# Performance work log

Hardware: AMD Instinct MI355X
Metric: run time of the kernel (lower is better)

Reference implementation:

```python
import jax, jax.numpy as jnp
import numpy as np

BETA = 0.25
B, N, D = 8, 4096, 256
NUM_CODES = 4096


def setup_inputs() -> dict:
    key = jax.random.key(0)
    kx, kc = jax.random.split(key)
    x = jax.random.normal(kx, (B, N, D), dtype=jnp.float32)
    # matches nn.init.uniform_(weight, -1/dim, 1/dim)
    codebook = jax.random.uniform(kc, (NUM_CODES, D), dtype=jnp.float32,
                                  minval=-1.0 / D, maxval=1.0 / D)
    return {"x": x, "codebook": codebook}


def reference(x, codebook):
    b, n, d = x.shape
    flat = x.reshape(b * n, d)                                   # [BN, D]
    # squared euclidean distances: ||z||^2 - 2 z.e^T + ||e||^2   # [BN, K]
    distances = (jnp.sum(flat * flat, axis=1, keepdims=True)
                 - 2.0 * jnp.einsum('md,kd->mk', flat, codebook)
                 + jnp.sum(codebook * codebook, axis=1)[None, :])
    indices = jnp.argmin(distances, axis=1)                      # [BN]
    z_q = codebook[indices].reshape(b, n, d)                     # [B, N, D]
    # commitment + codebook losses (detach == stop_gradient)
    sg = jax.lax.stop_gradient
    loss = jnp.mean((sg(z_q) - x) ** 2) + BETA * jnp.mean((z_q - sg(x)) ** 2)
    # straight-through estimator
    z_q_st = x + sg(z_q - x)
    return z_q_st, loss, indices.reshape(b, n)
```

## Files before the change

kernel.cpp:

```cpp
#include <hip/hip_runtime.h>

#define MTOT 32768
#define KC   4096
#define DDIM 256
#define BM   64
#define ZELEMS (MTOT * DDIM)
#define THRESH 2.0e-4f
#define WLCAP 8192
#define RGRID 2048

typedef _Float16 half8 __attribute__((ext_vector_type(8)));
typedef float f32x4 __attribute__((ext_vector_type(4)));

__device__ __forceinline__ void gload_lds16(const void* g, void* l) {
  __builtin_amdgcn_global_load_lds(
      (const __attribute__((address_space(1))) void*)g,
      (__attribute__((address_space(3))) void*)l, 16, 0, 0);
}

__device__ __forceinline__ float sqr_rn(float v) { return __fmul_rn(v, v); }

__global__ __launch_bounds__(256) void vq_prep2(const float* __restrict__ x,
                                                const float* __restrict__ cb,
                                                float* __restrict__ S,
                                                float* __restrict__ cnorm,
                                                _Float16* __restrict__ cbsw,
                                                int* __restrict__ wl_count,
                                                double* __restrict__ accum) {
  const int t = threadIdx.x;
  if (blockIdx.x == 0 && t == 0) { *accum = 0.0; *wl_count = 0; }
  const int sub = t >> 4, lane16 = t & 15;
  const int h = lane16 >> 3, j = lane16 & 7;
  const bool isrow = blockIdx.x < 2048;
  const int idx = (isrow ? blockIdx.x : blockIdx.x - 2048) * 16 + sub;
  const float* p = (isrow ? x + (size_t)idx * DDIM : cb + (size_t)idx * DDIM);

  float r = 0.f;
  const float* q = p + h * 128 + j;
#pragma unroll
  for (int i = 0; i < 16; ++i) r = __fadd_rn(r, sqr_rn(q[i * 8]));
  r = __fadd_rn(r, __shfl_xor(r, 1, 64));
  r = __fadd_rn(r, __shfl_xor(r, 2, 64));
  r = __fadd_rn(r, __shfl_xor(r, 4, 64));
  float sv = __fadd_rn(r, __shfl_xor(r, 8, 64));
  if (lane16 == 0) {
    if (isrow) S[idx] = sv; else cnorm[idx] = sv;
  }

  if (!isrow) {
    const int sw = idx & 7;
    _Float16* dst = cbsw + (size_t)idx * DDIM;
#pragma unroll
    for (int c = 0; c < 2; ++c) {
      int jj = lane16 + c * 16;
      float4 a4 = *reinterpret_cast<const float4*>(p + jj * 8);
      float4 b4 = *reinterpret_cast<const float4*>(p + jj * 8 + 4);
      union { half8 v; _Float16 hh[8]; } u;
      u.hh[0] = (_Float16)(a4.x * 256.0f); u.hh[1] = (_Float16)(a4.y * 256.0f);
      u.hh[2] = (_Float16)(a4.z * 256.0f); u.hh[3] = (_Float16)(a4.w * 256.0f);
      u.hh[4] = (_Float16)(b4.x * 256.0f); u.hh[5] = (_Float16)(b4.y * 256.0f);
      u.hh[6] = (_Float16)(b4.z * 256.0f); u.hh[7] = (_Float16)(b4.w * 256.0f);
      *reinterpret_cast<half8*>(dst + ((jj ^ sw) * 8)) = u.v;
    }
  }
}

__global__ __launch_bounds__(256, 2) void vq_score(const float* __restrict__ x,
                                                   const _Float16* __restrict__ cbsw,
                                                   const float* __restrict__ Sarr,
                                                   const float* __restrict__ cnorm,
                                                   int* __restrict__ bestidx,
                                                   int* __restrict__ wl,
                                                   int* __restrict__ wl_count,
                                                   double* __restrict__ accum) {
  __shared__ _Float16 cbt[4][2][4096];
  __shared__ float scrV1[4][BM];
  __shared__ float scrV2[4][BM];
  __shared__ int   scrI1[4][BM];

  const int t = threadIdx.x;
  const int m0 = blockIdx.x * BM;
  const int lane = t & 63, w = t >> 6;
  const int lo = lane & 15, hi = lane >> 4;

#pragma unroll
  for (int j = 0; j < 8; ++j)
    gload_lds16(cbsw + w * 4096 + j * 512 + lane * 8, &cbt[w][0][j * 512]);

  half8 a[4][8];
#pragma unroll
  for (int s2 = 0; s2 < 4; ++s2) {
    const float* xr = x + (size_t)(m0 + s2 * 16 + lo) * DDIM + hi * 8;
#pragma unroll
    for (int s = 0; s < 8; ++s) {
      float4 u0 = *reinterpret_cast<const float4*>(xr + s * 32);
      float4 u1 = *reinterpret_cast<const float4*>(xr + s * 32 + 4);
      union { half8 v; _Float16 h[8]; } uu;
      uu.h[0] = (_Float16)u0.x; uu.h[1] = (_Float16)u0.y;
      uu.h[2] = (_Float16)u0.z; uu.h[3] = (_Float16)u0.w;
      uu.h[4] = (_Float16)u1.x; uu.h[5] = (_Float16)u1.y;
      uu.h[6] = (_Float16)u1.z; uu.h[7] = (_Float16)u1.w;
      a[s2][s] = uu.v;
    }
  }

  const int code_l = w * 16 + lo;
  const int bswz = (lo & 7) << 3;

  float v1[4][4], v2[4][4]; int i1[4][4];
#pragma unroll
  for (int s2 = 0; s2 < 4; ++s2)
#pragma unroll
    for (int r = 0; r < 4; ++r) { v1[s2][r] = 3.4e38f; v2[s2][r] = 3.4e38f; i1[s2][r] = 0; }

  float Ccur = cnorm[code_l];

  for (int kt = 0; kt < KC / 64; ++kt) {
#pragma unroll
    for (int s2 = 0; s2 < 4; ++s2)
#pragma unroll
      for (int s = 0; s < 8; ++s)
        asm volatile("" : "+v"(a[s2][s]));

    const int cur = kt & 1;
    asm volatile("s_waitcnt vmcnt(0) lgkmcnt(0)" ::: "memory");
    if (kt < KC / 64 - 1) {
      const _Float16* src = cbsw + (size_t)(kt + 1) * 16384 + w * 4096 + lane * 8;
#pragma unroll
      for (int j = 0; j < 8; ++j)
        gload_lds16(src + j * 512, &cbt[w][cur ^ 1][j * 512]);
    }
    float Cnext = (kt < KC / 64 - 1) ? cnorm[(kt + 1) * 64 + code_l] : 0.f;

    f32x4 acc[4];
#pragma unroll
    for (int s2 = 0; s2 < 4; ++s2) acc[s2] = (f32x4){0.f, 0.f, 0.f, 0.f};
#pragma unroll
    for (int s = 0; s < 8; ++s) {
      half8 b = *reinterpret_cast<half8*>(
          &cbt[w][cur][(lo * 256 + s * 32 + hi * 8) ^ bswz]);
      acc[0] = __builtin_amdgcn_mfma_f32_16x16x32_f16(a[0][s], b, acc[0], 0, 0, 0);
      acc[1] = __builtin_amdgcn_mfma_f32_16x16x32_f16(a[1][s], b, acc[1], 0, 0, 0);
      acc[2] = __builtin_amdgcn_mfma_f32_16x16x32_f16(a[2][s], b, acc[2], 0, 0, 0);
      acc[3] = __builtin_amdgcn_mfma_f32_16x16x32_f16(a[3][s], b, acc[3], 0, 0, 0);
    }
    const int code = kt * 64 + code_l;
#pragma unroll
    for (int s2 = 0; s2 < 4; ++s2) {
#pragma unroll
      for (int r = 0; r < 4; ++r) {
        float sv = fmaf(acc[s2][r], -0.0078125f, Ccur);
        bool lt = sv < v1[s2][r];
        v2[s2][r] = fminf(v2[s2][r], lt ? v1[s2][r] : sv);
        if (lt) { v1[s2][r] = sv; i1[s2][r] = code; }
      }
    }
    Ccur = Cnext;
  }

#pragma unroll
  for (int s2 = 0; s2 < 4; ++s2) {
#pragma unroll
    for (int r = 0; r < 4; ++r) {
      float v = v1[s2][r], u = v2[s2][r]; int ii = i1[s2][r];
#pragma unroll
      for (int m = 1; m <= 8; m <<= 1) {
        float ov = __shfl_xor(v, m, 64);
        int   oi = __shfl_xor(ii, m, 64);
        float ou = __shfl_xor(u, m, 64);
        float mx = fmaxf(v, ov);
        u = fminf(fminf(u, ou), mx);
        bool take = (ov < v) || (ov == v && oi < ii);
        if (take) { v = ov; ii = oi; }
      }
      if (lo == 0) {
        int rowl = s2 * 16 + hi * 4 + r;
        scrV1[w][rowl] = v;
        scrV2[w][rowl] = u;
        scrI1[w][rowl] = ii;
      }
    }
  }
  __syncthreads();

  float part = 0.f;
  if (t < BM) {
    float bv1 = 3.4e38f, bv2 = 3.4e38f; int bi1 = 0x7fffffff;
#pragma unroll
    for (int c = 0; c < 4; ++c) {
      float v = scrV1[c][t];
      float u = scrV2[c][t];
      int  ii = scrI1[c][t];
      float mx = fmaxf(bv1, v);
      bv2 = fminf(fminf(bv2, u), mx);
      if (v < bv1 || (v == bv1 && ii < bi1)) { bv1 = v; bi1 = ii; }
    }
    int row = m0 + t;
    bestidx[row] = bi1;
    float gap = bv2 - bv1;
    if (gap <= THRESH) {
      int pos = atomicAdd(wl_count, 1);
      if (pos >= WLCAP) part = __fadd_rn(Sarr[row], bv1);
      else wl[pos] = row;
    } else {
      part = __fadd_rn(Sarr[row], bv1);
    }
  }
#pragma unroll
  for (int off = 32; off >= 1; off >>= 1) part += __shfl_down(part, off, 64);
  if (t == 0) atomicAdd(accum, (double)part);
}

__global__ __launch_bounds__(256) void vq_rescore(const float* __restrict__ x,
                                                  const float* __restrict__ cb,
                                                  const float* __restrict__ Sarr,
                                                  const float* __restrict__ cnorm,
                                                  const int* __restrict__ wl,
                                                  const int* __restrict__ wl_count,
                                                  float* __restrict__ pD,
                                                  int* __restrict__ pI) {
  const int cnt = min(*wl_count, WLCAP);
  if (cnt == 0) return;
  const int ngroups = (cnt + 3) >> 2;
  const int nitems = ngroups * 16;

  __shared__ float xs[4][260];
  __shared__ int rsh[4];
  __shared__ float scrv[4][4];
  __shared__ int   scri[4][4];

  const int t = threadIdx.x;
  const int lane = t & 63, w = t >> 6;

  for (int item = blockIdx.x; item < nitems; item += RGRID) {
    const int g = item >> 4, chunk = item & 15;
    __syncthreads();
    if (t < 4) { int e = g * 4 + t; rsh[t] = wl[(e < cnt) ? e : g * 4]; }
    __syncthreads();
    { int i = t >> 6, dq = t & 63;
      *reinterpret_cast<float4*>(&xs[i][dq * 4]) =
          *reinterpret_cast<const float4*>(x + (size_t)rsh[i] * DDIM + dq * 4); }
    __syncthreads();

    const int code = chunk * 256 + t;
    const float* cp = cb + (size_t)code * DDIM;
    const float C = cnorm[code];

    float acc[4][4];
#pragma unroll
    for (int i = 0; i < 4; ++i)
#pragma unroll
      for (int l = 0; l < 4; ++l) acc[i][l] = 0.f;

#pragma unroll 8
    for (int dq = 0; dq < 64; ++dq) {
      float4 cv = *reinterpret_cast<const float4*>(cp + dq * 4);
#pragma unroll
      for (int i = 0; i < 4; ++i) {
        float4 xv = *reinterpret_cast<float4*>(&xs[i][dq * 4]);
        acc[i][0] = __fadd_rn(acc[i][0], __fmul_rn(xv.x, cv.x));
        acc[i][1] = __fadd_rn(acc[i][1], __fmul_rn(xv.y, cv.y));
        acc[i][2] = __fadd_rn(acc[i][2], __fmul_rn(xv.z, cv.z));
        acc[i][3] = __fadd_rn(acc[i][3], __fmul_rn(xv.w, cv.w));
      }
    }

#pragma unroll
    for (int i = 0; i < 4; ++i) {
      float e = __fadd_rn(__fadd_rn(acc[i][0], acc[i][1]),
                          __fadd_rn(acc[i][2], acc[i][3]));
      float Sv = Sarr[rsh[i]];
      float D = __fadd_rn(__fsub_rn(Sv, __fmul_rn(2.0f, e)), C);
      float v = D; int ii = code;
#pragma unroll
      for (int m = 1; m <= 32; m <<= 1) {
        float ov = __shfl_xor(v, m, 64);
        int   oi = __shfl_xor(ii, m, 64);
        if (ov < v || (ov == v && oi < ii)) { v = ov; ii = oi; }
      }
      if (lane == 0) { scrv[i][w] = v; scri[i][w] = ii; }
    }
    __syncthreads();
    if (t < 4) {
      float bv = 3.4e38f; int bi = 0x7fffffff;
#pragma unroll
      for (int c = 0; c < 4; ++c) {
        float v = scrv[t][c]; int ii = scri[t][c];
        if (v < bv || (v == bv && ii < bi)) { bv = v; bi = ii; }
      }
      int rpos = g * 4 + t;
      if (rpos < cnt) { pD[rpos * 16 + chunk] = bv; pI[rpos * 16 + chunk] = bi; }
    }
  }
}

__global__ __launch_bounds__(256) void vq_combine(const int* __restrict__ wl,
                                                  const int* __restrict__ wl_count,
                                                  const float* __restrict__ pD,
                                                  const int* __restrict__ pI,
                                                  int* __restrict__ bestidx,
                                                  double* __restrict__ accum) {
  const int cnt = min(*wl_count, WLCAP);
  for (int r = blockIdx.x * 256 + threadIdx.x; r < cnt; r += gridDim.x * 256) {
    float bv = 3.4e38f; int bi = 0x7fffffff;
#pragma unroll
    for (int c = 0; c < 16; ++c) {
      float v = pD[r * 16 + c]; int ii = pI[r * 16 + c];
      if (v < bv || (v == bv && ii < bi)) { bv = v; bi = ii; }
    }
    bestidx[wl[r]] = bi;
    atomicAdd(accum, (double)bv);
  }
}

__global__ __launch_bounds__(256) void vq_emit(const float* __restrict__ x,
                                               const float* __restrict__ cb,
                                               const int* __restrict__ bestidx,
                                               float* __restrict__ out) {
  __shared__ int ish[64];
  const int t = threadIdx.x;
  const int m0 = blockIdx.x * 64;
  if (t < 64) {
    int ii = bestidx[m0 + t];
    ish[t] = ii;
    out[(size_t)ZELEMS + 1 + m0 + t] = (float)ii;
  }
  __syncthreads();
#pragma unroll
  for (int i = 0; i < 16; ++i) {
    int fi = t + i * 256;
    int row = fi >> 6, dc = fi & 63;
    int code = ish[row];
    float4 c4 = *reinterpret_cast<const float4*>(cb + (size_t)code * DDIM + dc * 4);
    float4 x4 = *reinterpret_cast<const float4*>(x + (size_t)(m0 + row) * DDIM + dc * 4);
    float4 o;
    o.x = __fadd_rn(x4.x, __fsub_rn(c4.x, x4.x));
    o.y = __fadd_rn(x4.y, __fsub_rn(c4.y, x4.y));
    o.z = __fadd_rn(x4.z, __fsub_rn(c4.z, x4.z));
    o.w = __fadd_rn(x4.w, __fsub_rn(c4.w, x4.w));
    *reinterpret_cast<float4*>(out + (size_t)(m0 + row) * DDIM + dc * 4) = o;
  }
}

__global__ void vq_final(const double* __restrict__ accum, float* __restrict__ out) {
  out[ZELEMS] = (float)(1.25 * accum[0] / (double)ZELEMS);
}

extern "C" void kernel_launch(void* const* d_in, const int* in_sizes, int n_in,
                              void* d_out, int out_size, void* d_ws, size_t ws_size,
                              hipStream_t stream) {
  const float* x  = (const float*)d_in[0];
  const float* cb = (const float*)d_in[1];
  float* out = (float*)d_out;

  char* ws = (char*)d_ws;
  float*     S        = (float*)(ws + 0);
  float*     cnorm    = (float*)(ws + 131072);
  int*       bestidx  = (int*)  (ws + 147456);
  int*       wl       = (int*)  (ws + 278528);
  int*       wl_count = (int*)  (ws + 311296);
  double*    accum    = (double*)(ws + 311312);
  float*     pD       = (float*)(ws + 315392);
  int*       pI       = (int*)  (ws + 839680);
  _Float16*  cbsw     = (_Float16*)(ws + 1363968);

  vq_prep2<<<2304, 256, 0, stream>>>(x, cb, S, cnorm, cbsw, wl_count, accum);
  vq_score<<<MTOT / BM, 256, 0, stream>>>(x, cbsw, S, cnorm, bestidx, wl, wl_count, accum);
  vq_rescore<<<RGRID, 256, 0, stream>>>(x, cb, S, cnorm, wl, wl_count, pD, pI);
  vq_combine<<<8, 256, 0, stream>>>(wl, wl_count, pD, pI, bestidx, accum);
  vq_emit<<<MTOT / 64, 256, 0, stream>>>(x, cb, bestidx, out);
  vq_final<<<1, 1, 0, stream>>>(accum, out);
}
```

Measured before the change: 186.4 us.

## Load codebook fragments directly from global into registers, dropping LDS staging

```diff
diff --git a/kernel.cpp b/kernel.cpp
--- a/kernel.cpp
+++ b/kernel.cpp
@@ -11,12 +11,6 @@
 
 typedef _Float16 half8 __attribute__((ext_vector_type(8)));
 typedef float f32x4 __attribute__((ext_vector_type(4)));
-
-__device__ __forceinline__ void gload_lds16(const void* g, void* l) {
-  __builtin_amdgcn_global_load_lds(
-      (const __attribute__((address_space(1))) void*)g,
-      (__attribute__((address_space(3))) void*)l, 16, 0, 0);
-}
 
 __device__ __forceinline__ float sqr_rn(float v) { return __fmul_rn(v, v); }
 
@@ -48,11 +42,12 @@
   }
 
   if (!isrow) {
-    const int sw = idx & 7;
-    _Float16* dst = cbsw + (size_t)idx * DDIM;
+    const int kt = idx >> 6, code_l = idx & 63;
+    _Float16* dst0 = cbsw + (size_t)kt * 16384 + code_l * 32;
 #pragma unroll
     for (int c = 0; c < 2; ++c) {
       int jj = lane16 + c * 16;
+      int s = jj >> 2, hi = jj & 3;
       float4 a4 = *reinterpret_cast<const float4*>(p + jj * 8);
       float4 b4 = *reinterpret_cast<const float4*>(p + jj * 8 + 4);
       union { half8 v; _Float16 hh[8]; } u;
@@ -60,7 +55,7 @@
       u.hh[2] = (_Float16)(a4.z * 256.0f); u.hh[3] = (_Float16)(a4.w * 256.0f);
       u.hh[4] = (_Float16)(b4.x * 256.0f); u.hh[5] = (_Float16)(b4.y * 256.0f);
       u.hh[6] = (_Float16)(b4.z * 256.0f); u.hh[7] = (_Float16)(b4.w * 256.0f);
-      *reinterpret_cast<half8*>(dst + ((jj ^ sw) * 8)) = u.v;
+      *reinterpret_cast<half8*>(dst0 + s * 2048 + hi * 8) = u.v;
     }
   }
 }
@@ -73,7 +68,6 @@
                                                    int* __restrict__ wl,
                                                    int* __restrict__ wl_count,
                                                    double* __restrict__ accum) {
-  __shared__ _Float16 cbt[4][2][4096];
   __shared__ float scrV1[4][BM];
   __shared__ float scrV2[4][BM];
   __shared__ int   scrI1[4][BM];
@@ -82,10 +76,6 @@
   const int m0 = blockIdx.x * BM;
   const int lane = t & 63, w = t >> 6;
   const int lo = lane & 15, hi = lane >> 4;
-
-#pragma unroll
-  for (int j = 0; j < 8; ++j)
-    gload_lds16(cbsw + w * 4096 + j * 512 + lane * 8, &cbt[w][0][j * 512]);
 
   half8 a[4][8];
 #pragma unroll
@@ -105,7 +95,7 @@
   }
 
   const int code_l = w * 16 + lo;
-  const int bswz = (lo & 7) << 3;
+  const _Float16* bb = cbsw + w * 512 + lo * 32 + hi * 8;
 
   float v1[4][4], v2[4][4]; int i1[4][4];
 #pragma unroll
@@ -115,35 +105,41 @@
 
   float Ccur = cnorm[code_l];
 
+#define BLOAD(dst, kt, s) \
+  dst = *reinterpret_cast<const half8*>(bb + ((size_t)(kt) * 8 + (s)) * 2048)
+#define QMFMA(buf, s0) \
+  do { \
+    acc[0] = __builtin_amdgcn_mfma_f32_16x16x32_f16(a[0][s0],     buf[0], acc[0], 0, 0, 0); \
+    acc[1] = __builtin_amdgcn_mfma_f32_16x16x32_f16(a[1][s0],     buf[0], acc[1], 0, 0, 0); \
+    acc[2] = __builtin_amdgcn_mfma_f32_16x16x32_f16(a[2][s0],     buf[0], acc[2], 0, 0, 0); \
+    acc[3] = __builtin_amdgcn_mfma_f32_16x16x32_f16(a[3][s0],     buf[0], acc[3], 0, 0, 0); \
+    acc[0] = __builtin_amdgcn_mfma_f32_16x16x32_f16(a[0][s0 + 1], buf[1], acc[0], 0, 0, 0); \
+    acc[1] = __builtin_amdgcn_mfma_f32_16x16x32_f16(a[1][s0 + 1], buf[1], acc[1], 0, 0, 0); \
+    acc[2] = __builtin_amdgcn_mfma_f32_16x16x32_f16(a[2][s0 + 1], buf[1], acc[2], 0, 0, 0); \
+    acc[3] = __builtin_amdgcn_mfma_f32_16x16x32_f16(a[3][s0 + 1], buf[1], acc[3], 0, 0, 0); \
+  } while (0)
+
+  half8 bufA[2], bufB[2];
+  BLOAD(bufA[0], 0, 0);
+  BLOAD(bufA[1], 0, 1);
+
   for (int kt = 0; kt < KC / 64; ++kt) {
-#pragma unroll
-    for (int s2 = 0; s2 < 4; ++s2)
-#pragma unroll
-      for (int s = 0; s < 8; ++s)
-        asm volatile("" : "+v"(a[s2][s]));
-
-    const int cur = kt & 1;
-    asm volatile("s_waitcnt vmcnt(0) lgkmcnt(0)" ::: "memory");
-    if (kt < KC / 64 - 1) {
-      const _Float16* src = cbsw + (size_t)(kt + 1) * 16384 + w * 4096 + lane * 8;
-#pragma unroll
-      for (int j = 0; j < 8; ++j)
-        gload_lds16(src + j * 512, &cbt[w][cur ^ 1][j * 512]);
-    }
-    float Cnext = (kt < KC / 64 - 1) ? cnorm[(kt + 1) * 64 + code_l] : 0.f;
+    const int ktn = (kt + 1) & 63;
+    float Cnext = cnorm[ktn * 64 + code_l];
 
     f32x4 acc[4];
 #pragma unroll
     for (int s2 = 0; s2 < 4; ++s2) acc[s2] = (f32x4){0.f, 0.f, 0.f, 0.f};
-#pragma unroll
-    for (int s = 0; s < 8; ++s) {
-      half8 b = *reinterpret_cast<half8*>(
-          &cbt[w][cur][(lo * 256 + s * 32 + hi * 8) ^ bswz]);
-      acc[0] = __builtin_amdgcn_mfma_f32_16x16x32_f16(a[0][s], b, acc[0], 0, 0, 0);
-      acc[1] = __builtin_amdgcn_mfma_f32_16x16x32_f16(a[1][s], b, acc[1], 0, 0, 0);
-      acc[2] = __builtin_amdgcn_mfma_f32_16x16x32_f16(a[2][s], b, acc[2], 0, 0, 0);
-      acc[3] = __builtin_amdgcn_mfma_f32_16x16x32_f16(a[3][s], b, acc[3], 0, 0, 0);
-    }
+
+    BLOAD(bufB[0], kt, 2);  BLOAD(bufB[1], kt, 3);
+    QMFMA(bufA, 0);
+    BLOAD(bufA[0], kt, 4);  BLOAD(bufA[1], kt, 5);
+    QMFMA(bufB, 2);
+    BLOAD(bufB[0], kt, 6);  BLOAD(bufB[1], kt, 7);
+    QMFMA(bufA, 4);
+    BLOAD(bufA[0], ktn, 0); BLOAD(bufA[1], ktn, 1);
+    QMFMA(bufB, 6);
+
     const int code = kt * 64 + code_l;
 #pragma unroll
     for (int s2 = 0; s2 < 4; ++s2) {
@@ -157,6 +153,8 @@
     }
     Ccur = Cnext;
   }
+#undef BLOAD
+#undef QMFMA
 
 #pragma unroll
   for (int s2 = 0; s2 < 4; ++s2) {
```

New measurement: 198.4 us. 1.06x slower.

## Share codebook tiles across two row groups in 512-thread score blocks

Applied to the files above, without the earlier changes.

```diff
diff --git a/kernel.cpp b/kernel.cpp
--- a/kernel.cpp
+++ b/kernel.cpp
@@ -3,7 +3,7 @@
 #define MTOT 32768
 #define KC   4096
 #define DDIM 256
-#define BM   64
+#define BM   128
 #define ZELEMS (MTOT * DDIM)
 #define THRESH 2.0e-4f
 #define WLCAP 8192
@@ -65,7 +65,7 @@
   }
 }
 
-__global__ __launch_bounds__(256, 2) void vq_score(const float* __restrict__ x,
+__global__ __launch_bounds__(512, 2) void vq_score(const float* __restrict__ x,
                                                    const _Float16* __restrict__ cbsw,
                                                    const float* __restrict__ Sarr,
                                                    const float* __restrict__ cnorm,
@@ -73,24 +73,39 @@
                                                    int* __restrict__ wl,
                                                    int* __restrict__ wl_count,
                                                    double* __restrict__ accum) {
-  __shared__ _Float16 cbt[4][2][4096];
+  __shared__ _Float16 cbt[2][64 * DDIM];
+  __shared__ float cn[KC];
   __shared__ float scrV1[4][BM];
   __shared__ float scrV2[4][BM];
   __shared__ int   scrI1[4][BM];
+  __shared__ float wred[8];
 
   const int t = threadIdx.x;
   const int m0 = blockIdx.x * BM;
   const int lane = t & 63, w = t >> 6;
+  const int rg = w >> 2, cg = w & 3;
   const int lo = lane & 15, hi = lane >> 4;
 
 #pragma unroll
-  for (int j = 0; j < 8; ++j)
-    gload_lds16(cbsw + w * 4096 + j * 512 + lane * 8, &cbt[w][0][j * 512]);
+  for (int j = 0; j < 4; ++j)
+    gload_lds16(cbsw + 0 * 16384 + w * 2048 + j * 512 + lane * 8,
+                &cbt[0][w * 2048 + j * 512]);
+#pragma unroll
+  for (int j = 0; j < 4; ++j)
+    gload_lds16(cbsw + 1 * 16384 + w * 2048 + j * 512 + lane * 8,
+                &cbt[1][w * 2048 + j * 512]);
+
+#pragma unroll
+  for (int i = 0; i < 2; ++i) {
+    int fi = t + i * 512;
+    *reinterpret_cast<float4*>(&cn[fi * 4]) =
+        *reinterpret_cast<const float4*>(cnorm + fi * 4);
+  }
 
   half8 a[4][8];
 #pragma unroll
   for (int s2 = 0; s2 < 4; ++s2) {
-    const float* xr = x + (size_t)(m0 + s2 * 16 + lo) * DDIM + hi * 8;
+    const float* xr = x + (size_t)(m0 + rg * 64 + s2 * 16 + lo) * DDIM + hi * 8;
 #pragma unroll
     for (int s = 0; s < 8; ++s) {
       float4 u0 = *reinterpret_cast<const float4*>(xr + s * 32);
@@ -104,7 +119,7 @@
     }
   }
 
-  const int code_l = w * 16 + lo;
+  const int code_l = cg * 16 + lo;
   const int bswz = (lo & 7) << 3;
 
   float v1[4][4], v2[4][4]; int i1[4][4];
@@ -113,32 +128,22 @@
 #pragma unroll
     for (int r = 0; r < 4; ++r) { v1[s2][r] = 3.4e38f; v2[s2][r] = 3.4e38f; i1[s2][r] = 0; }
 
-  float Ccur = cnorm[code_l];
+  __syncthreads();
 
   for (int kt = 0; kt < KC / 64; ++kt) {
-#pragma unroll
-    for (int s2 = 0; s2 < 4; ++s2)
-#pragma unroll
-      for (int s = 0; s < 8; ++s)
-        asm volatile("" : "+v"(a[s2][s]));
-
     const int cur = kt & 1;
-    asm volatile("s_waitcnt vmcnt(0) lgkmcnt(0)" ::: "memory");
-    if (kt < KC / 64 - 1) {
-      const _Float16* src = cbsw + (size_t)(kt + 1) * 16384 + w * 4096 + lane * 8;
-#pragma unroll
-      for (int j = 0; j < 8; ++j)
-        gload_lds16(src + j * 512, &cbt[w][cur ^ 1][j * 512]);
-    }
-    float Cnext = (kt < KC / 64 - 1) ? cnorm[(kt + 1) * 64 + code_l] : 0.f;
-
+    if (kt < KC / 64 - 1) asm volatile("s_waitcnt vmcnt(4)" ::: "memory");
+    else                  asm volatile("s_waitcnt vmcnt(0)" ::: "memory");
+    __builtin_amdgcn_s_barrier();
+
+    const float C = cn[kt * 64 + code_l];
     f32x4 acc[4];
 #pragma unroll
     for (int s2 = 0; s2 < 4; ++s2) acc[s2] = (f32x4){0.f, 0.f, 0.f, 0.f};
 #pragma unroll
     for (int s = 0; s < 8; ++s) {
       half8 b = *reinterpret_cast<half8*>(
-          &cbt[w][cur][(lo * 256 + s * 32 + hi * 8) ^ bswz]);
+          &cbt[cur][(code_l * DDIM + s * 32 + hi * 8) ^ bswz]);
       acc[0] = __builtin_amdgcn_mfma_f32_16x16x32_f16(a[0][s], b, acc[0], 0, 0, 0);
       acc[1] = __builtin_amdgcn_mfma_f32_16x16x32_f16(a[1][s], b, acc[1], 0, 0, 0);
       acc[2] = __builtin_amdgcn_mfma_f32_16x16x32_f16(a[2][s], b, acc[2], 0, 0, 0);
@@ -149,13 +154,21 @@
     for (int s2 = 0; s2 < 4; ++s2) {
 #pragma unroll
       for (int r = 0; r < 4; ++r) {
-        float sv = fmaf(acc[s2][r], -0.0078125f, Ccur);
+        float sv = fmaf(acc[s2][r], -0.0078125f, C);
+        float mx = fmaxf(v1[s2][r], sv);
+        v2[s2][r] = fminf(v2[s2][r], mx);
         bool lt = sv < v1[s2][r];
-        v2[s2][r] = fminf(v2[s2][r], lt ? v1[s2][r] : sv);
         if (lt) { v1[s2][r] = sv; i1[s2][r] = code; }
       }
     }
-    Ccur = Cnext;
+
+    __builtin_amdgcn_s_barrier();
+    if (kt < KC / 64 - 2) {
+#pragma unroll
+      for (int j = 0; j < 4; ++j)
+        gload_lds16(cbsw + (size_t)(kt + 2) * 16384 + w * 2048 + j * 512 + lane * 8,
+                    &cbt[cur][w * 2048 + j * 512]);
+    }
   }
 
 #pragma unroll
@@ -174,10 +187,10 @@
         if (take) { v = ov; ii = oi; }
       }
       if (lo == 0) {
-        int rowl = s2 * 16 + hi * 4 + r;
-        scrV1[w][rowl] = v;
-        scrV2[w][rowl] = u;
-        scrI1[w][rowl] = ii;
+        int rowl = rg * 64 + s2 * 16 + hi * 4 + r;
+        scrV1[cg][rowl] = v;
+        scrV2[cg][rowl] = u;
+        scrI1[cg][rowl] = ii;
       }
     }
   }
@@ -208,7 +221,14 @@
   }
 #pragma unroll
   for (int off = 32; off >= 1; off >>= 1) part += __shfl_down(part, off, 64);
-  if (t == 0) atomicAdd(accum, (double)part);
+  if (lane == 0) wred[w] = part;
+  __syncthreads();
+  if (t == 0) {
+    double s = 0.0;
+#pragma unroll
+    for (int i = 0; i < 8; ++i) s += (double)wred[i];
+    atomicAdd(accum, s);
+  }
 }
 
 __global__ __launch_bounds__(256) void vq_rescore(const float* __restrict__ x,
@@ -365,7 +385,7 @@
   _Float16*  cbsw     = (_Float16*)(ws + 1363968);
 
   vq_prep2<<<2304, 256, 0, stream>>>(x, cb, S, cnorm, cbsw, wl_count, accum);
-  vq_score<<<MTOT / BM, 256, 0, stream>>>(x, cbsw, S, cnorm, bestidx, wl, wl_count, accum);
+  vq_score<<<MTOT / BM, 512, 0, stream>>>(x, cbsw, S, cnorm, bestidx, wl, wl_count, accum);
   vq_rescore<<<RGRID, 256, 0, stream>>>(x, cb, S, cnorm, wl, wl_count, pD, pI);
   vq_combine<<<8, 256, 0, stream>>>(wl, wl_count, pD, pI, bestidx, accum);
   vq_emit<<<MTOT / 64, 256, 0, stream>>>(x, cb, bestidx, out);
```

New measurement: 176.8 us. 1.05x faster.
